# Kernel tuning notes

Measured on AMD Instinct MI355X. Metric: run time of the kernel, lower is better.

Reference implementation:

```python
import jax, jax.numpy as jnp
import numpy as np

WH, WW = 8, 8
NUM_HEADS = 12
DIM = 384
N = WH * WW

def _rel_pos_index():
    # Swin relative position index, static [N, N] int array
    coords = np.stack(np.meshgrid(np.arange(WH), np.arange(WW), indexing='ij'))  # [2, wh, ww]
    cf = coords.reshape(2, -1)                      # [2, N]
    rel = cf[:, :, None] - cf[:, None, :]           # [2, N, N]
    rel = rel.transpose(1, 2, 0).copy()             # [N, N, 2]
    rel[..., 0] += WH - 1
    rel[..., 1] += WW - 1
    rel[..., 0] *= 2 * WW - 1
    return jnp.asarray(rel.sum(-1))                 # [N, N]

REL_IDX = _rel_pos_index()


def setup_inputs() -> dict:
    key = jax.random.key(0)
    ks = jax.random.split(key, 4)
    Bn = 4096
    x = jax.random.normal(ks[0], (Bn, N, DIM), dtype=jnp.float32)
    qkv_w = jax.random.normal(ks[1], (3 * DIM, DIM), dtype=jnp.float32) * 0.02
    qkv_b = jnp.zeros((3 * DIM,), dtype=jnp.float32)
    proj_w = jax.random.normal(ks[2], (DIM, DIM), dtype=jnp.float32) * 0.02
    proj_b = jnp.zeros((DIM,), dtype=jnp.float32)
    bias_table = jax.random.normal(ks[3], ((2 * WH - 1) * (2 * WW - 1), NUM_HEADS), dtype=jnp.float32) * 0.02
    return {"x": x, "qkv_w": qkv_w, "qkv_b": qkv_b, "proj_w": proj_w, "proj_b": proj_b, "bias_table": bias_table}


def reference(x, qkv_w, qkv_b, proj_w, proj_b, bias_table):
    Bn, n, C = x.shape
    H = NUM_HEADS
    hd = C // H
    scale = hd ** (-0.5)
    qkv = (x @ qkv_w.T + qkv_b).reshape(Bn, n, 3, H, hd)
    q = qkv[:, :, 0].transpose(0, 2, 1, 3)  # [Bn, H, n, hd]
    k = qkv[:, :, 1].transpose(0, 2, 1, 3)
    v = qkv[:, :, 2].transpose(0, 2, 1, 3)
    attn = jnp.einsum('bhqd,bhkd->bhqk', q, k) * scale  # [Bn, H, n, n]
    bias = bias_table[REL_IDX]                           # [n, n, H]
    attn = attn + bias.transpose(2, 0, 1)[None]          # add rel-pos bias
    attn = jax.nn.softmax(attn, axis=-1)
    out = jnp.einsum('bhqk,bhkd->bqhd', attn, v).reshape(Bn, n, C)
    return out @ proj_w.T + proj_b
```

## Files before the change

### kernel.cpp

```cpp
#include <hip/hip_runtime.h>

#define NT 64
#define NH 12
#define HD 32
#define DIM 384
#define NWIN 4096
#define TPB 512
#define PTPB 256

typedef __bf16 bf16;
typedef __bf16 bf16x8 __attribute__((ext_vector_type(8)));
typedef float floatx4 __attribute__((ext_vector_type(4)));

__device__ __align__(16) bf16 g_wqkv[3 * DIM * DIM];
__device__ __align__(16) bf16 g_wproj[DIM * DIM];
__device__ __align__(16) float g_biasF[NH * NT * NT];

__global__ void convert_weights(const float* __restrict__ qkv_w,
                                const float* __restrict__ proj_w,
                                const float* __restrict__ bias_table) {
    int i = blockIdx.x * blockDim.x + threadIdx.x;
    if (i < 3 * DIM * DIM) g_wqkv[i] = (bf16)qkv_w[i];
    if (i < DIM * DIM)     g_wproj[i] = (bf16)proj_w[i];
    if (i < NH * NT * NT) {
        int h = i >> 12, qk = i & 4095;
        int q = qk >> 6, kv = qk & 63;
        int idx = ((q >> 3) - (kv >> 3) + 7) * 15 + ((q & 7) - (kv & 7) + 7);
        g_biasF[i] = bias_table[idx * NH + h];
    }
}

__device__ inline bf16x8 load_cvt8(const float* p) {
    float4 f0 = *(const float4*)p;
    float4 f1 = *(const float4*)(p + 4);
    bf16x8 a;
    a[0] = (bf16)f0.x; a[1] = (bf16)f0.y; a[2] = (bf16)f0.z; a[3] = (bf16)f0.w;
    a[4] = (bf16)f1.x; a[5] = (bf16)f1.y; a[6] = (bf16)f1.z; a[7] = (bf16)f1.w;
    return a;
}

__global__ __launch_bounds__(TPB, 4) void attn_kernel(
    const float* __restrict__ x,
    const float* __restrict__ qkv_b,
    float* __restrict__ out)
{
    __shared__ __align__(16) char smem[73728];
    bf16 (*sq)[2][64][40] = (bf16(*)[2][64][40])smem;
    bf16 (*sk)[2][64][40] = (bf16(*)[2][64][40])(smem + 20480);
    bf16* svT = (bf16*)(smem + 40960);
    bf16* sP  = (bf16*)(smem + 57344);

    const int t    = threadIdx.x;
    const int win  = blockIdx.x;
    const int wave = t >> 6;
    const int lane = t & 63;
    const int quad = lane >> 4;
    const int l15  = lane & 15;
    const int mt   = wave & 3;
    const int grp  = wave >> 2;

    const float* xw = x + (size_t)win * (NT * DIM);
    bf16x8 afrag[12];
    #pragma unroll
    for (int ks = 0; ks < 12; ++ks)
        afrag[ks] = load_cvt8(xw + (mt * 16 + l15) * DIM + ks * 32 + quad * 8);

    const float scale = 0.17677669529663687f;
    float* outw = out + (size_t)win * (NT * DIM);
    bf16* const sPw = sP + wave * 1024;

    #pragma unroll 1
    for (int hp = 0; hp < NH / 2; ++hp) {
        const int buf = hp & 1;

        #pragma unroll
        for (int jj = 0; jj < 6; ++jj) {
            const int hl  = jj / 3;
            const int nt  = grp * 3 + (jj % 3);
            const int s   = nt >> 1;
            const int nhh = (nt & 1) * 16;
            const int h   = hp * 2 + hl;
            const int wrow = s * DIM + h * HD + nhh + l15;
            const bf16* Wp = g_wqkv + (size_t)wrow * DIM + quad * 8;
            bf16x8 b0[6], b1[6];
            #pragma unroll
            for (int i = 0; i < 6; ++i) b0[i] = *(const bf16x8*)(Wp + i * 32);
            #pragma unroll
            for (int i = 0; i < 6; ++i) b1[i] = *(const bf16x8*)(Wp + 192 + i * 32);
            floatx4 acc0 = {0.f, 0.f, 0.f, 0.f}, acc1 = {0.f, 0.f, 0.f, 0.f};
            #pragma unroll
            for (int i = 0; i < 6; ++i) {
                acc0 = __builtin_amdgcn_mfma_f32_16x16x32_bf16(afrag[i],     b0[i], acc0, 0, 0, 0);
                acc1 = __builtin_amdgcn_mfma_f32_16x16x32_bf16(afrag[6 + i], b1[i], acc1, 0, 0, 0);
            }
            const float bv = qkv_b[wrow];
            #pragma unroll
            for (int r = 0; r < 4; ++r) {
                const int m = mt * 16 + quad * 4 + r;
                const float v = acc0[r] + acc1[r] + bv;
                if (s == 0)      sq[buf][hl][m][nhh + l15] = (bf16)(v * scale);
                else if (s == 1) sk[buf][hl][m][nhh + l15] = (bf16)v;
                else {
                    const int row = nhh + l15;
                    svT[(buf * 2 + hl) * 2048 + row * 64 + (m ^ ((row & 7) << 3))] = (bf16)v;
                }
            }
        }
        __syncthreads();

        const int h = hp * 2 + grp;
        const float* bias = g_biasF + h * (NT * NT) + (mt * 16 + quad * 4) * NT + l15;
        float bb[4][4];
        #pragma unroll
        for (int jt = 0; jt < 4; ++jt)
            #pragma unroll
            for (int r = 0; r < 4; ++r)
                bb[jt][r] = bias[r * NT + jt * 16];

        const bf16x8 aq = *(const bf16x8*)&sq[buf][grp][mt * 16 + l15][quad * 8];
        floatx4 sc[4];
        #pragma unroll
        for (int jt = 0; jt < 4; ++jt) {
            const bf16x8 bk = *(const bf16x8*)&sk[buf][grp][jt * 16 + l15][quad * 8];
            floatx4 z = {0.f, 0.f, 0.f, 0.f};
            sc[jt] = __builtin_amdgcn_mfma_f32_16x16x32_bf16(aq, bk, z, 0, 0, 0);
        }
        #pragma unroll
        for (int jt = 0; jt < 4; ++jt)
            #pragma unroll
            for (int r = 0; r < 4; ++r)
                sc[jt][r] += bb[jt][r];

        float mx[4], sm[4], inv[4];
        #pragma unroll
        for (int r = 0; r < 4; ++r) {
            mx[r] = fmaxf(fmaxf(sc[0][r], sc[1][r]), fmaxf(sc[2][r], sc[3][r]));
            mx[r] = fmaxf(mx[r], __shfl_xor(mx[r], 1));
            mx[r] = fmaxf(mx[r], __shfl_xor(mx[r], 2));
            mx[r] = fmaxf(mx[r], __shfl_xor(mx[r], 4));
            mx[r] = fmaxf(mx[r], __shfl_xor(mx[r], 8));
        }
        float e[4][4];
        #pragma unroll
        for (int jt = 0; jt < 4; ++jt)
            #pragma unroll
            for (int r = 0; r < 4; ++r)
                e[jt][r] = __expf(sc[jt][r] - mx[r]);
        #pragma unroll
        for (int r = 0; r < 4; ++r) {
            sm[r] = (e[0][r] + e[1][r]) + (e[2][r] + e[3][r]);
            sm[r] += __shfl_xor(sm[r], 1);
            sm[r] += __shfl_xor(sm[r], 2);
            sm[r] += __shfl_xor(sm[r], 4);
            sm[r] += __shfl_xor(sm[r], 8);
            inv[r] = 1.0f / sm[r];
        }
        #pragma unroll
        for (int jt = 0; jt < 4; ++jt)
            #pragma unroll
            for (int r = 0; r < 4; ++r) {
                const int row = quad * 4 + r;
                const int col = jt * 16 + l15;
                sPw[row * 64 + (col ^ ((row & 7) << 3))] = (bf16)(e[jt][r] * inv[r]);
            }

        bf16x8 ap[2];
        #pragma unroll
        for (int ks = 0; ks < 2; ++ks)
            ap[ks] = *(const bf16x8*)&sPw[l15 * 64 + ((ks * 32 + quad * 8) ^ ((l15 & 7) << 3))];
        const bf16* vb = svT + (buf * 2 + grp) * 2048;
        #pragma unroll
        for (int pnt = 0; pnt < 2; ++pnt) {
            floatx4 acc = {0.f, 0.f, 0.f, 0.f};
            #pragma unroll
            for (int ks = 0; ks < 2; ++ks) {
                const int vrow = pnt * 16 + l15;
                const bf16x8 bv = *(const bf16x8*)&vb[vrow * 64 + ((ks * 32 + quad * 8) ^ ((vrow & 7) << 3))];
                acc = __builtin_amdgcn_mfma_f32_16x16x32_bf16(ap[ks], bv, acc, 0, 0, 0);
            }
            #pragma unroll
            for (int r = 0; r < 4; ++r)
                outw[(size_t)(mt * 16 + quad * 4 + r) * DIM + h * HD + pnt * 16 + l15] = acc[r];
        }
    }
}

__global__ __launch_bounds__(PTPB, 4) void proj_kernel(
    const float* __restrict__ proj_b,
    float* __restrict__ out)
{
    const int t    = threadIdx.x;
    const int wave = t >> 6;
    const int lane = t & 63;
    const int quad = lane >> 4;
    const int l15  = lane & 15;
    float* base = out + (size_t)blockIdx.x * (NT * DIM);

    bf16x8 afrag[12];
    #pragma unroll
    for (int ks = 0; ks < 12; ++ks)
        afrag[ks] = load_cvt8(base + (wave * 16 + l15) * DIM + ks * 32 + quad * 8);

    #pragma unroll
    for (int nt = 0; nt < DIM / 16; ++nt) {
        const bf16* Wp = g_wproj + (size_t)(nt * 16 + l15) * DIM + quad * 8;
        bf16x8 b0[6], b1[6];
        #pragma unroll
        for (int i = 0; i < 6; ++i) b0[i] = *(const bf16x8*)(Wp + i * 32);
        #pragma unroll
        for (int i = 0; i < 6; ++i) b1[i] = *(const bf16x8*)(Wp + 192 + i * 32);
        floatx4 acc0 = {0.f, 0.f, 0.f, 0.f}, acc1 = {0.f, 0.f, 0.f, 0.f};
        #pragma unroll
        for (int i = 0; i < 6; ++i) {
            acc0 = __builtin_amdgcn_mfma_f32_16x16x32_bf16(afrag[i],     b0[i], acc0, 0, 0, 0);
            acc1 = __builtin_amdgcn_mfma_f32_16x16x32_bf16(afrag[6 + i], b1[i], acc1, 0, 0, 0);
        }
        const float pb = proj_b[nt * 16 + l15];
        #pragma unroll
        for (int r = 0; r < 4; ++r)
            base[(size_t)(wave * 16 + quad * 4 + r) * DIM + nt * 16 + l15] = acc0[r] + acc1[r] + pb;
    }
}

extern "C" void kernel_launch(void* const* d_in, const int* in_sizes, int n_in,
                              void* d_out, int out_size, void* d_ws, size_t ws_size,
                              hipStream_t stream) {
    const float* x          = (const float*)d_in[0];
    const float* qkv_w      = (const float*)d_in[1];
    const float* qkv_b      = (const float*)d_in[2];
    const float* proj_w     = (const float*)d_in[3];
    const float* proj_b     = (const float*)d_in[4];
    const float* bias_table = (const float*)d_in[5];
    float* out = (float*)d_out;

    convert_weights<<<dim3((3 * DIM * DIM + 255) / 256), dim3(256), 0, stream>>>(qkv_w, proj_w, bias_table);
    attn_kernel<<<dim3(NWIN), dim3(TPB), 0, stream>>>(x, qkv_b, out);
    proj_kernel<<<dim3(NWIN), dim3(PTPB), 0, stream>>>(proj_b, out);
}
```

Measured before the change: 2.763 ms.

## Stage x tile in swizzled LDS and double-buffer weight fragments in both GEMMs

Both kernels now convert the fp32 input window to bf16 once into a swizzled shared-memory tile. The QKV and projection GEMMs then read A fragments from LDS instead of holding them in registers. Each wave now owns whole weight column tiles and reuses each loaded B fragment across two or four M-tiles, with ping-pong register buffers overlapping weight loads with MFMA. The per-head double-buffering of Q/K/V is dropped in favour of extra barriers, and LDS use grows while proj occupancy drops to 3, which may reduce latency hiding.

```diff
diff --git a/kernel.cpp b/kernel.cpp
--- a/kernel.cpp
+++ b/kernel.cpp
@@ -30,13 +30,11 @@
     }
 }
 
-__device__ inline bf16x8 load_cvt8(const float* p) {
-    float4 f0 = *(const float4*)p;
-    float4 f1 = *(const float4*)(p + 4);
-    bf16x8 a;
-    a[0] = (bf16)f0.x; a[1] = (bf16)f0.y; a[2] = (bf16)f0.z; a[3] = (bf16)f0.w;
-    a[4] = (bf16)f1.x; a[5] = (bf16)f1.y; a[6] = (bf16)f1.z; a[7] = (bf16)f1.w;
-    return a;
+__device__ inline bf16x8 sx_ld(const char* base, int row, int colE) {
+    return *(const bf16x8*)(base + row * 768 + (((colE) * 2) ^ ((row & 7) << 4)));
+}
+__device__ inline void sx_st(char* base, int row, int colE, bf16x8 v) {
+    *(bf16x8*)(base + row * 768 + (((colE) * 2) ^ ((row & 7) << 4))) = v;
 }
 
 __global__ __launch_bounds__(TPB, 4) void attn_kernel(
@@ -44,11 +42,11 @@
     const float* __restrict__ qkv_b,
     float* __restrict__ out)
 {
-    __shared__ __align__(16) char smem[73728];
-    bf16 (*sq)[2][64][40] = (bf16(*)[2][64][40])smem;
-    bf16 (*sk)[2][64][40] = (bf16(*)[2][64][40])(smem + 20480);
-    bf16* svT = (bf16*)(smem + 40960);
-    bf16* sP  = (bf16*)(smem + 57344);
+    __shared__ __align__(16) char smem[77824];
+    bf16 (*sq)[64][40] = (bf16(*)[64][40])(smem + 49152);
+    bf16 (*sk)[64][40] = (bf16(*)[64][40])(smem + 59392);
+    bf16* svT = (bf16*)(smem + 69632);
+    bf16* sP  = (bf16*)(smem + 49152);
 
     const int t    = threadIdx.x;
     const int win  = blockIdx.x;
@@ -59,11 +57,21 @@
     const int mt   = wave & 3;
     const int grp  = wave >> 2;
 
-    const float* xw = x + (size_t)win * (NT * DIM);
-    bf16x8 afrag[12];
-    #pragma unroll
-    for (int ks = 0; ks < 12; ++ks)
-        afrag[ks] = load_cvt8(xw + (mt * 16 + l15) * DIM + ks * 32 + quad * 8);
+    {
+        const float4* src = (const float4*)(x + (size_t)win * (NT * DIM));
+        #pragma unroll
+        for (int it = 0; it < (NT * DIM / 8) / TPB; ++it) {
+            int i = t + it * TPB;
+            float4 f0 = src[i * 2];
+            float4 f1 = src[i * 2 + 1];
+            int r = i / 48, c8 = (i % 48) * 8;
+            bf16x8 v8;
+            v8[0] = (bf16)f0.x; v8[1] = (bf16)f0.y; v8[2] = (bf16)f0.z; v8[3] = (bf16)f0.w;
+            v8[4] = (bf16)f1.x; v8[5] = (bf16)f1.y; v8[6] = (bf16)f1.z; v8[7] = (bf16)f1.w;
+            sx_st(smem, r, c8, v8);
+        }
+    }
+    __syncthreads();
 
     const float scale = 0.17677669529663687f;
     float* outw = out + (size_t)win * (NT * DIM);
@@ -71,41 +79,54 @@
 
     #pragma unroll 1
     for (int hp = 0; hp < NH / 2; ++hp) {
-        const int buf = hp & 1;
-
-        #pragma unroll
-        for (int jj = 0; jj < 6; ++jj) {
-            const int hl  = jj / 3;
-            const int nt  = grp * 3 + (jj % 3);
-            const int s   = nt >> 1;
-            const int nhh = (nt & 1) * 16;
-            const int h   = hp * 2 + hl;
-            const int wrow = s * DIM + h * HD + nhh + l15;
+        bf16x8 bA[12], bB[12];
+
+        auto loadB = [&](bf16x8* b, int id) {
+            int nt = id >> 1;
+            int hl = nt / 6, nt6 = nt % 6;
+            int s = nt6 >> 1, nhh = (nt6 & 1) * 16;
+            int wrow = s * DIM + (hp * 2 + hl) * HD + nhh + l15;
             const bf16* Wp = g_wqkv + (size_t)wrow * DIM + quad * 8;
-            bf16x8 b0[6], b1[6];
-            #pragma unroll
-            for (int i = 0; i < 6; ++i) b0[i] = *(const bf16x8*)(Wp + i * 32);
-            #pragma unroll
-            for (int i = 0; i < 6; ++i) b1[i] = *(const bf16x8*)(Wp + 192 + i * 32);
+            #pragma unroll
+            for (int ks = 0; ks < 12; ++ks) b[ks] = *(const bf16x8*)(Wp + ks * 32);
+        };
+        auto computeStore = [&](const bf16x8* b, int id) {
+            int nt = id >> 1, mh = id & 1;
+            int hl = nt / 6, nt6 = nt % 6;
+            int s = nt6 >> 1, nhh = (nt6 & 1) * 16;
+            int wrow = s * DIM + (hp * 2 + hl) * HD + nhh + l15;
+            float bv = qkv_b[wrow];
             floatx4 acc0 = {0.f, 0.f, 0.f, 0.f}, acc1 = {0.f, 0.f, 0.f, 0.f};
             #pragma unroll
-            for (int i = 0; i < 6; ++i) {
-                acc0 = __builtin_amdgcn_mfma_f32_16x16x32_bf16(afrag[i],     b0[i], acc0, 0, 0, 0);
-                acc1 = __builtin_amdgcn_mfma_f32_16x16x32_bf16(afrag[6 + i], b1[i], acc1, 0, 0, 0);
-            }
-            const float bv = qkv_b[wrow];
-            #pragma unroll
-            for (int r = 0; r < 4; ++r) {
-                const int m = mt * 16 + quad * 4 + r;
-                const float v = acc0[r] + acc1[r] + bv;
-                if (s == 0)      sq[buf][hl][m][nhh + l15] = (bf16)(v * scale);
-                else if (s == 1) sk[buf][hl][m][nhh + l15] = (bf16)v;
-                else {
-                    const int row = nhh + l15;
-                    svT[(buf * 2 + hl) * 2048 + row * 64 + (m ^ ((row & 7) << 3))] = (bf16)v;
+            for (int ks = 0; ks < 12; ++ks) {
+                bf16x8 a0 = sx_ld(smem, mh * 32 + l15,      ks * 32 + quad * 8);
+                bf16x8 a1 = sx_ld(smem, mh * 32 + 16 + l15, ks * 32 + quad * 8);
+                acc0 = __builtin_amdgcn_mfma_f32_16x16x32_bf16(a0, b[ks], acc0, 0, 0, 0);
+                acc1 = __builtin_amdgcn_mfma_f32_16x16x32_bf16(a1, b[ks], acc1, 0, 0, 0);
+            }
+            #pragma unroll
+            for (int im = 0; im < 2; ++im) {
+                const floatx4& acc = im ? acc1 : acc0;
+                #pragma unroll
+                for (int r = 0; r < 4; ++r) {
+                    int m = mh * 32 + im * 16 + quad * 4 + r;
+                    float v = acc[r] + bv;
+                    if (s == 0)      sq[hl][m][nhh + l15] = (bf16)(v * scale);
+                    else if (s == 1) sk[hl][m][nhh + l15] = (bf16)v;
+                    else {
+                        int row = nhh + l15;
+                        svT[hl * 2048 + row * 64 + (m ^ ((row & 7) << 3))] = (bf16)v;
+                    }
                 }
             }
-        }
+        };
+
+        loadB(bA, wave);
+        loadB(bB, wave + 8);
+        computeStore(bA, wave);
+        loadB(bA, wave + 16);
+        computeStore(bB, wave + 8);
+        computeStore(bA, wave + 16);
         __syncthreads();
 
         const int h = hp * 2 + grp;
@@ -117,11 +138,11 @@
             for (int r = 0; r < 4; ++r)
                 bb[jt][r] = bias[r * NT + jt * 16];
 
-        const bf16x8 aq = *(const bf16x8*)&sq[buf][grp][mt * 16 + l15][quad * 8];
+        const bf16x8 aq = *(const bf16x8*)&sq[grp][mt * 16 + l15][quad * 8];
         floatx4 sc[4];
         #pragma unroll
         for (int jt = 0; jt < 4; ++jt) {
-            const bf16x8 bk = *(const bf16x8*)&sk[buf][grp][jt * 16 + l15][quad * 8];
+            const bf16x8 bk = *(const bf16x8*)&sk[grp][jt * 16 + l15][quad * 8];
             floatx4 z = {0.f, 0.f, 0.f, 0.f};
             sc[jt] = __builtin_amdgcn_mfma_f32_16x16x32_bf16(aq, bk, z, 0, 0, 0);
         }
@@ -155,6 +176,8 @@
             sm[r] += __shfl_xor(sm[r], 8);
             inv[r] = 1.0f / sm[r];
         }
+        __syncthreads();
+
         #pragma unroll
         for (int jt = 0; jt < 4; ++jt)
             #pragma unroll
@@ -168,7 +191,7 @@
         #pragma unroll
         for (int ks = 0; ks < 2; ++ks)
             ap[ks] = *(const bf16x8*)&sPw[l15 * 64 + ((ks * 32 + quad * 8) ^ ((l15 & 7) << 3))];
-        const bf16* vb = svT + (buf * 2 + grp) * 2048;
+        const bf16* vb = svT + grp * 2048;
         #pragma unroll
         for (int pnt = 0; pnt < 2; ++pnt) {
             floatx4 acc = {0.f, 0.f, 0.f, 0.f};
@@ -182,13 +205,15 @@
             for (int r = 0; r < 4; ++r)
                 outw[(size_t)(mt * 16 + quad * 4 + r) * DIM + h * HD + pnt * 16 + l15] = acc[r];
         }
-    }
-}
-
-__global__ __launch_bounds__(PTPB, 4) void proj_kernel(
+        __syncthreads();
+    }
+}
+
+__global__ __launch_bounds__(PTPB, 3) void proj_kernel(
     const float* __restrict__ proj_b,
     float* __restrict__ out)
 {
+    __shared__ __align__(16) char smem[49152];
     const int t    = threadIdx.x;
     const int wave = t >> 6;
     const int lane = t & 63;
@@ -196,30 +221,61 @@
     const int l15  = lane & 15;
     float* base = out + (size_t)blockIdx.x * (NT * DIM);
 
-    bf16x8 afrag[12];
-    #pragma unroll
-    for (int ks = 0; ks < 12; ++ks)
-        afrag[ks] = load_cvt8(base + (wave * 16 + l15) * DIM + ks * 32 + quad * 8);
-
-    #pragma unroll
-    for (int nt = 0; nt < DIM / 16; ++nt) {
+    {
+        const float4* src = (const float4*)base;
+        #pragma unroll
+        for (int it = 0; it < (NT * DIM / 8) / PTPB; ++it) {
+            int i = t + it * PTPB;
+            float4 f0 = src[i * 2];
+            float4 f1 = src[i * 2 + 1];
+            int r = i / 48, c8 = (i % 48) * 8;
+            bf16x8 v8;
+            v8[0] = (bf16)f0.x; v8[1] = (bf16)f0.y; v8[2] = (bf16)f0.z; v8[3] = (bf16)f0.w;
+            v8[4] = (bf16)f1.x; v8[5] = (bf16)f1.y; v8[6] = (bf16)f1.z; v8[7] = (bf16)f1.w;
+            sx_st(smem, r, c8, v8);
+        }
+    }
+    __syncthreads();
+
+    bf16x8 bA[12], bB[12];
+    auto loadB = [&](bf16x8* b, int nt) {
         const bf16* Wp = g_wproj + (size_t)(nt * 16 + l15) * DIM + quad * 8;
-        bf16x8 b0[6], b1[6];
-        #pragma unroll
-        for (int i = 0; i < 6; ++i) b0[i] = *(const bf16x8*)(Wp + i * 32);
-        #pragma unroll
-        for (int i = 0; i < 6; ++i) b1[i] = *(const bf16x8*)(Wp + 192 + i * 32);
-        floatx4 acc0 = {0.f, 0.f, 0.f, 0.f}, acc1 = {0.f, 0.f, 0.f, 0.f};
-        #pragma unroll
-        for (int i = 0; i < 6; ++i) {
-            acc0 = __builtin_amdgcn_mfma_f32_16x16x32_bf16(afrag[i],     b0[i], acc0, 0, 0, 0);
-            acc1 = __builtin_amdgcn_mfma_f32_16x16x32_bf16(afrag[6 + i], b1[i], acc1, 0, 0, 0);
-        }
-        const float pb = proj_b[nt * 16 + l15];
-        #pragma unroll
-        for (int r = 0; r < 4; ++r)
-            base[(size_t)(wave * 16 + quad * 4 + r) * DIM + nt * 16 + l15] = acc0[r] + acc1[r] + pb;
-    }
+        #pragma unroll
+        for (int ks = 0; ks < 12; ++ks) b[ks] = *(const bf16x8*)(Wp + ks * 32);
+    };
+    auto computeStore = [&](const bf16x8* b, int nt) {
+        floatx4 a0 = {0.f,0.f,0.f,0.f}, a1 = {0.f,0.f,0.f,0.f},
+                a2 = {0.f,0.f,0.f,0.f}, a3 = {0.f,0.f,0.f,0.f};
+        #pragma unroll
+        for (int ks = 0; ks < 12; ++ks) {
+            bf16x8 f0 = sx_ld(smem, 0  + l15, ks * 32 + quad * 8);
+            bf16x8 f1 = sx_ld(smem, 16 + l15, ks * 32 + quad * 8);
+            bf16x8 f2 = sx_ld(smem, 32 + l15, ks * 32 + quad * 8);
+            bf16x8 f3 = sx_ld(smem, 48 + l15, ks * 32 + quad * 8);
+            a0 = __builtin_amdgcn_mfma_f32_16x16x32_bf16(f0, b[ks], a0, 0, 0, 0);
+            a1 = __builtin_amdgcn_mfma_f32_16x16x32_bf16(f1, b[ks], a1, 0, 0, 0);
+            a2 = __builtin_amdgcn_mfma_f32_16x16x32_bf16(f2, b[ks], a2, 0, 0, 0);
+            a3 = __builtin_amdgcn_mfma_f32_16x16x32_bf16(f3, b[ks], a3, 0, 0, 0);
+        }
+        float pb = proj_b[nt * 16 + l15];
+        #pragma unroll
+        for (int r = 0; r < 4; ++r) {
+            base[(size_t)(0  + quad * 4 + r) * DIM + nt * 16 + l15] = a0[r] + pb;
+            base[(size_t)(16 + quad * 4 + r) * DIM + nt * 16 + l15] = a1[r] + pb;
+            base[(size_t)(32 + quad * 4 + r) * DIM + nt * 16 + l15] = a2[r] + pb;
+            base[(size_t)(48 + quad * 4 + r) * DIM + nt * 16 + l15] = a3[r] + pb;
+        }
+    };
+
+    const int n0 = wave * 6;
+    loadB(bA, n0 + 0);
+    loadB(bB, n0 + 1);
+    computeStore(bA, n0 + 0); loadB(bA, n0 + 2);
+    computeStore(bB, n0 + 1); loadB(bB, n0 + 3);
+    computeStore(bA, n0 + 2); loadB(bA, n0 + 4);
+    computeStore(bB, n0 + 3); loadB(bB, n0 + 5);
+    computeStore(bA, n0 + 4);
+    computeStore(bB, n0 + 5);
 }
 
 extern "C" void kernel_launch(void* const* d_in, const int* in_sizes, int n_in,
```

Measured after the change: 3.020 ms. +9.3%, slower.
